# Kernel tuning notes

Measured on AMD Instinct MI355X. Metric: run time of the kernel, lower is better.

## Reference

```python
import jax, jax.numpy as jnp
import numpy as np

B, S, D, H = 2, 2048, 1024, 16
DH = D // H


def setup_inputs() -> dict:
    key = jax.random.key(0)
    ks_ = jax.random.split(key, 12)
    s = 1.0 / np.sqrt(D)
    return {
        "qs": jax.random.normal(ks_[0], (B, S, D), jnp.float32),
        "ks": jax.random.normal(ks_[1], (B, S, D), jnp.float32),
        "vs": jax.random.normal(ks_[2], (B, S, D), jnp.float32),
        "mask": jax.random.randint(ks_[3], (B, S), 0, 2) > 0,
        "Wq": jax.random.normal(ks_[4], (D, D), jnp.float32) * s,
        "bq": jnp.zeros((D,), jnp.float32),
        "Wk": jax.random.normal(ks_[5], (D, D), jnp.float32) * s,
        "bk": jnp.zeros((D,), jnp.float32),
        "Wv": jax.random.normal(ks_[6], (D, D), jnp.float32) * s,
        "bv": jnp.zeros((D,), jnp.float32),
        "Wo": jax.random.normal(ks_[7], (D, D), jnp.float32) * s,
        "bo": jnp.zeros((D,), jnp.float32),
    }


def reference(qs, ks, vs, mask, Wq, bq, Wk, bk, Wv, bv, Wo, bo):
    # Linear projections (single-layer MLPs)
    q = qs @ Wq + bq  # [B,S,D]
    k = ks @ Wk + bk
    v = vs @ Wv + bv
    # split heads: B L (H D) -> B H L D
    split = lambda x: x.reshape(B, S, H, DH).transpose(0, 2, 1, 3)
    q, k, v = split(q), split(k), split(v)
    scores = jnp.einsum("bhqd,bhkd->bhqk", q, k) / jnp.sqrt(jnp.float32(DH))
    scores = jnp.where(mask[:, None, None, :], scores, -jnp.inf)
    attn = jax.nn.softmax(scores, axis=-1)  # [B,H,Q,K]
    ctx = jnp.einsum("bhqk,bhkd->bhqd", attn, v)
    ctx = ctx.transpose(0, 2, 1, 3).reshape(B, S, D)  # B H L D -> B L (H D)
    out = ctx @ Wo + bo
    return (out, attn)
```

## Files before the change

kernel.cpp:

```cpp
#include <hip/hip_runtime.h>
#include <hip/hip_bf16.h>
#include <cstdint>

#define NBATCH 2
#define NS 2048
#define NDIM 1024
#define NHEAD 16
#define NDH 64
#define NBH 32

typedef __bf16 bf16x8 __attribute__((ext_vector_type(8)));
typedef float f32x4 __attribute__((ext_vector_type(4)));

#define QK_EXP2_SCALE 0.1803368801111244f

#define WAITV(N) asm volatile("s_waitcnt vmcnt(" #N ")" ::: "memory")
#define FENCE asm volatile("" ::: "memory")

static __device__ __forceinline__ f32x4 mfma16(bf16x8 a, bf16x8 b, f32x4 c) {
  return __builtin_amdgcn_mfma_f32_16x16x32_bf16(a, b, c, 0, 0, 0);
}

static __device__ __forceinline__ void gload_lds16(const void* g, void* l) {
  __builtin_amdgcn_global_load_lds(
      (const __attribute__((address_space(1))) uint32_t*)g,
      (__attribute__((address_space(3))) uint32_t*)l, 16, 0, 0);
}

__global__ __launch_bounds__(256) void k_cvt_x(const float* __restrict__ q,
                                               const float* __restrict__ k,
                                               const float* __restrict__ v,
                                               __bf16* __restrict__ out) {
  const float* src = blockIdx.y == 0 ? q : (blockIdx.y == 1 ? k : v);
  __bf16* dst = out + (size_t)blockIdx.y * (size_t)(4096 * 1024);
  int i = blockIdx.x * 256 + threadIdx.x;
  const float4* s4 = reinterpret_cast<const float4*>(src) + (size_t)i * 2;
  float4 a = s4[0], b = s4[1];
  bf16x8 o;
  o[0] = (__bf16)a.x; o[1] = (__bf16)a.y; o[2] = (__bf16)a.z; o[3] = (__bf16)a.w;
  o[4] = (__bf16)b.x; o[5] = (__bf16)b.y; o[6] = (__bf16)b.z; o[7] = (__bf16)b.w;
  *reinterpret_cast<bf16x8*>(dst + (size_t)i * 8) = o;
}

__global__ __launch_bounds__(256) void k_cvt_w(const float* __restrict__ Wq,
                                               const float* __restrict__ Wk,
                                               const float* __restrict__ Wv,
                                               const float* __restrict__ Wo,
                                               __bf16* __restrict__ out,
                                               const int* __restrict__ mask,
                                               float* __restrict__ biasf) {
  if (blockIdx.y == 4) {
    int t = blockIdx.x * 256 + threadIdx.x;
    if (t < NBATCH * NS) biasf[t] = mask[t] ? 0.f : -1e30f;
    return;
  }
  const float* W = blockIdx.y == 0 ? Wq : (blockIdx.y == 1 ? Wk
                   : (blockIdx.y == 2 ? Wv : Wo));
  __bf16* dst = out + (size_t)blockIdx.y * (size_t)(1024 * 1024);
  int t = blockIdx.x * 256 + threadIdx.x;
  int n = t & 1023;
  int kc = t >> 10;
  bf16x8 o;
#pragma unroll
  for (int j = 0; j < 8; ++j) o[j] = (__bf16)W[(size_t)(kc * 8 + j) * 1024 + n];
  *reinterpret_cast<bf16x8*>(dst + (size_t)n * 1024 + kc * 8) = o;
}

__global__ __launch_bounds__(256) void k_tr_v(const __bf16* __restrict__ V,
                                              __bf16* __restrict__ Vt) {
  int t = blockIdx.x * 256 + threadIdx.x;
  int d = t & 63;
  int sc = (t >> 6) & 255;
  int bh = t >> 14;
  bf16x8 o;
#pragma unroll
  for (int j = 0; j < 8; ++j)
    o[j] = V[((size_t)bh * 2048 + sc * 8 + j) * 64 + d];
  *reinterpret_cast<bf16x8*>(Vt + ((size_t)bh * 64 + d) * 2048 + sc * 8) = o;
}

__global__ __launch_bounds__(256) void k_gemm(const __bf16* __restrict__ Abase,
                                              const __bf16* __restrict__ Btbase,
                                              const float* __restrict__ b0,
                                              const float* __restrict__ b1,
                                              const float* __restrict__ b2,
                                              void* __restrict__ outbase,
                                              int mode) {
  __shared__ __align__(16) char smem[65536];
  const int job = blockIdx.y;
  const __bf16* A = Abase + (size_t)job * (size_t)(4096 * 1024);
  const __bf16* Bt = Btbase + (size_t)job * (size_t)(1024 * 1024);
  const float* bias = job == 0 ? b0 : (job == 1 ? b1 : b2);
  const int x = blockIdx.x;
  const int mt = (x & 7) * 4 + (x >> 6);
  const int nt = (x >> 3) & 7;
  const int tid = threadIdx.x;
  const int w = tid >> 6, l = tid & 63;
  const int wr = w >> 1, wc = w & 1;

  auto stage = [&](int buf, int kt) {
    const int k0 = kt * 64;
    char* al = smem + buf * 32768;
    char* bl = al + 16384;
#pragma unroll
    for (int i = 0; i < 4; ++i) {
      int ch = tid + i * 256;
      int r = ch >> 3, c = ch & 7;
      int cs = c ^ (r & 7);
      gload_lds16(A + (size_t)(mt * 128 + r) * 1024 + k0 + cs * 8, al + ch * 16);
      gload_lds16(Bt + (size_t)(nt * 128 + r) * 1024 + k0 + cs * 8, bl + ch * 16);
    }
  };

  f32x4 acc[4][4] = {};
  stage(0, 0);
  for (int kt = 0; kt < 16; ++kt) {
    __syncthreads();
    if (kt + 1 < 16) stage((kt + 1) & 1, kt + 1);
    const char* al = smem + (kt & 1) * 32768;
    const char* bl = al + 16384;
#pragma unroll
    for (int ks = 0; ks < 2; ++ks) {
      bf16x8 af[4], bfr[4];
#pragma unroll
      for (int i = 0; i < 4; ++i) {
        int ra = wr * 64 + i * 16 + (l & 15);
        int ca = (ks * 4 + (l >> 4)) ^ (ra & 7);
        af[i] = *reinterpret_cast<const bf16x8*>(al + ra * 128 + ca * 16);
        int rb = wc * 64 + i * 16 + (l & 15);
        int cb = (ks * 4 + (l >> 4)) ^ (rb & 7);
        bfr[i] = *reinterpret_cast<const bf16x8*>(bl + rb * 128 + cb * 16);
      }
#pragma unroll
      for (int mi = 0; mi < 4; ++mi)
#pragma unroll
        for (int ni = 0; ni < 4; ++ni)
          acc[mi][ni] = mfma16(af[mi], bfr[ni], acc[mi][ni]);
    }
  }

  if (mode == 0) {
    const float sc = (job == 0) ? QK_EXP2_SCALE : 1.0f;
    __bf16* outp = (__bf16*)outbase + (size_t)job * (size_t)(NBH * NS * NDH);
#pragma unroll
    for (int mi = 0; mi < 4; ++mi)
#pragma unroll
      for (int ni = 0; ni < 4; ++ni)
#pragma unroll
        for (int r = 0; r < 4; ++r) {
          int m = mt * 128 + wr * 64 + mi * 16 + (l >> 4) * 4 + r;
          int n = nt * 128 + wc * 64 + ni * 16 + (l & 15);
          float v = (acc[mi][ni][r] + bias[n]) * sc;
          int b = m >> 11, s = m & 2047, h = n >> 6, d = n & 63;
          outp[(((size_t)(b * 16 + h)) * 2048 + s) * 64 + d] = (__bf16)v;
        }
  } else {
    float* outp = (float*)outbase;
#pragma unroll
    for (int mi = 0; mi < 4; ++mi)
#pragma unroll
      for (int ni = 0; ni < 4; ++ni)
#pragma unroll
        for (int r = 0; r < 4; ++r) {
          int m = mt * 128 + wr * 64 + mi * 16 + (l >> 4) * 4 + r;
          int n = nt * 128 + wc * 64 + ni * 16 + (l & 15);
          outp[(size_t)m * 1024 + n] = acc[mi][ni][r] + bias[n];
        }
  }
}

__global__ __launch_bounds__(256, 2) void k_attn(
    const __bf16* __restrict__ Qw, const __bf16* __restrict__ Kw,
    const __bf16* __restrict__ Vt, const float* __restrict__ biasf,
    float* __restrict__ attn_out, __bf16* __restrict__ ctx_out) {
  __shared__ __align__(16) char smem[75264];
  const int wg = blockIdx.x;
  const int swz = (wg & 7) * 64 + (wg >> 3);
  const int qt = swz & 15;
  const int bh = swz >> 4;
  const int b = bh >> 4;
  const int tid = threadIdx.x, w = tid >> 6, l = tid & 63;
  const int g = l >> 4, c = l & 15;
  const int qw = qt * 128 + w * 32;
  const float* biasb = biasf + b * 2048;

  bf16x8 qa[2][2];
#pragma unroll
  for (int mi = 0; mi < 2; ++mi)
#pragma unroll
    for (int ks = 0; ks < 2; ++ks)
      qa[mi][ks] = *reinterpret_cast<const bf16x8*>(
          Qw + ((size_t)bh * 2048 + qw + mi * 16 + c) * 64 + ks * 32 + g * 8);

  auto stageK = [&](char* dst, int kt) {
#pragma unroll
    for (int i = 0; i < 4; ++i) {
      int ch = tid + i * 256;
      int r = ch >> 3, cc = ch & 7;
      int cs = cc ^ (r & 7);
      gload_lds16(Kw + ((size_t)bh * 2048 + kt * 128 + r) * 64 + cs * 8,
                  dst + ch * 16);
    }
  };
  auto stageV = [&](char* dst, int kt) {
#pragma unroll
    for (int i = 0; i < 4; ++i) {
      int ch = tid + i * 256;
      int r = ch >> 4, cc = ch & 15;
      int cs = cc ^ (r & 15);
      gload_lds16(Vt + ((size_t)bh * 64 + r) * 2048 + kt * 128 + cs * 8,
                  dst + ch * 16);
    }
  };
  auto stageBias = [&](int slot, int kt) {
    if (l < 32)
      gload_lds16(biasb + kt * 128 + l * 4, smem + 73728 + slot * 512);
  };

  float rs[2] = {0.f, 0.f};
  stageK(smem, 0);
  stageBias(0, 0);
  int sl = 0;
  for (int kt = 0; kt < 16; ++kt) {
    int nx = (sl + 1 == 3) ? 0 : sl + 1;
    if (kt + 1 < 16) {
      stageK(smem + nx * 16384, kt + 1);
      stageBias(nx, kt + 1);
      WAITV(5);
    } else {
      WAITV(0);
    }
    __builtin_amdgcn_s_barrier();
    FENCE;
    const char* kl = smem + sl * 16384;
    const float* bl = (const float*)(smem + 73728 + sl * 512);
#pragma unroll
    for (int nb = 0; nb < 8; ++nb) {
      bf16x8 kb[2];
#pragma unroll
      for (int ks = 0; ks < 2; ++ks) {
        int r = nb * 16 + c;
        int cc = (ks * 4 + g) ^ (r & 7);
        kb[ks] = *reinterpret_cast<const bf16x8*>(kl + r * 128 + cc * 16);
      }
      f32x4 cinit = *reinterpret_cast<const f32x4*>(bl + nb * 16 + g * 4);
#pragma unroll
      for (int mi = 0; mi < 2; ++mi) {
        f32x4 s = mfma16(kb[0], qa[mi][0], cinit);
        s = mfma16(kb[1], qa[mi][1], s);
        rs[mi] += exp2f(s[0]) + exp2f(s[1]) + exp2f(s[2]) + exp2f(s[3]);
      }
    }
    sl = nx;
  }
  float inv_[2];
#pragma unroll
  for (int mi = 0; mi < 2; ++mi) {
    float v = rs[mi];
    v += __shfl_xor(v, 16, 64);
    v += __shfl_xor(v, 32, 64);
    inv_[mi] = v > 0.f ? 1.f / v : 0.f;
  }
  FENCE; __builtin_amdgcn_s_barrier(); FENCE;

  f32x4 ctx[2][4] = {};
  float* attnb = attn_out + (size_t)bh * 2048 * 2048;
  char* pF = smem + 65536 + w * 2048;
  stageK(smem, 0);
  stageV(smem + 32768, 0);
  stageBias(0, 0);
  for (int kt = 0; kt < 16; ++kt) {
    if (kt + 1 < 16) {
      int nx3 = (kt + 1) % 3;
      stageK(smem + ((kt + 1) & 1) * 16384, kt + 1);
      stageV(smem + 32768 + ((kt + 1) & 1) * 16384, kt + 1);
      stageBias(nx3, kt + 1);
    }
    if (kt == 0) WAITV(9);
    else if (kt == 15) WAITV(16);
    else WAITV(25);
    FENCE; __builtin_amdgcn_s_barrier(); FENCE;
    const char* kl = smem + (kt & 1) * 16384;
    const char* vl = smem + 32768 + (kt & 1) * 16384;
    const float* bl = (const float*)(smem + 73728 + (kt % 3) * 512);
#pragma unroll
    for (int kc = 0; kc < 4; ++kc) {
      bf16x8 kbj[2][2];
      f32x4 cin[2];
#pragma unroll
      for (int j = 0; j < 2; ++j) {
        const int nb = kc * 2 + j;
#pragma unroll
        for (int ks = 0; ks < 2; ++ks) {
          int r = nb * 16 + c;
          int cc = (ks * 4 + g) ^ (r & 7);
          kbj[j][ks] = *reinterpret_cast<const bf16x8*>(kl + r * 128 + cc * 16);
        }
        cin[j] = *reinterpret_cast<const f32x4*>(bl + nb * 16 + g * 4);
      }
      bf16x8 vb[4];
#pragma unroll
      for (int nd = 0; nd < 4; ++nd) {
        int dd = nd * 16 + c;
        int ch = (kc * 4 + g) ^ (dd & 15);
        vb[nd] = *reinterpret_cast<const bf16x8*>(vl + dd * 256 + ch * 16);
      }
#pragma unroll
      for (int mi = 0; mi < 2; ++mi) {
#pragma unroll
        for (int j = 0; j < 2; ++j) {
          f32x4 s = mfma16(kbj[j][0], qa[mi][0], cin[j]);
          s = mfma16(kbj[j][1], qa[mi][1], s);
          f32x4 p;
#pragma unroll
          for (int r = 0; r < 4; ++r) p[r] = exp2f(s[r]) * inv_[mi];
          *reinterpret_cast<f32x4*>(
              pF + c * 128 + (((j * 4 + g) ^ (c & 7)) * 16)) = p;
        }
        bf16x8 pa;
        {
          f32x4 lo = *reinterpret_cast<const f32x4*>(
              pF + c * 128 + (((2 * g) ^ (c & 7)) * 16));
          f32x4 hi = *reinterpret_cast<const f32x4*>(
              pF + c * 128 + (((2 * g + 1) ^ (c & 7)) * 16));
          pa[0] = (__bf16)lo[0]; pa[1] = (__bf16)lo[1];
          pa[2] = (__bf16)lo[2]; pa[3] = (__bf16)lo[3];
          pa[4] = (__bf16)hi[0]; pa[5] = (__bf16)hi[1];
          pa[6] = (__bf16)hi[2]; pa[7] = (__bf16)hi[3];
        }
#pragma unroll
        for (int nd = 0; nd < 4; ++nd)
          ctx[mi][nd] = mfma16(pa, vb[nd], ctx[mi][nd]);
#pragma unroll
        for (int u = 0; u < 2; ++u) {
          int rr = u * 8 + (l >> 3);
          int ch = (l & 7) ^ (rr & 7);
          f32x4 pv = *reinterpret_cast<const f32x4*>(pF + rr * 128 + ch * 16);
          *reinterpret_cast<f32x4*>(
              attnb + (size_t)(qw + mi * 16 + rr) * 2048 + kt * 128 +
              kc * 32 + (l & 7) * 4) = pv;
        }
      }
    }
    FENCE; __builtin_amdgcn_s_barrier(); FENCE;
  }

  const int h = bh & 15;
#pragma unroll
  for (int mi = 0; mi < 2; ++mi)
#pragma unroll
    for (int nd = 0; nd < 4; ++nd)
#pragma unroll
      for (int r = 0; r < 4; ++r) {
        int m = b * 2048 + qw + mi * 16 + g * 4 + r;
        int n = h * 64 + nd * 16 + c;
        ctx_out[(size_t)m * 1024 + n] = (__bf16)ctx[mi][nd][r];
      }
}

extern "C" void kernel_launch(void* const* d_in, const int* in_sizes, int n_in,
                              void* d_out, int out_size, void* d_ws,
                              size_t ws_size, hipStream_t stream) {
  const float* qs = (const float*)d_in[0];
  const float* ks = (const float*)d_in[1];
  const float* vs = (const float*)d_in[2];
  const int* mask = (const int*)d_in[3];
  const float* Wq = (const float*)d_in[4];
  const float* bq = (const float*)d_in[5];
  const float* Wk = (const float*)d_in[6];
  const float* bk = (const float*)d_in[7];
  const float* Wv = (const float*)d_in[8];
  const float* bv = (const float*)d_in[9];
  const float* Wo = (const float*)d_in[10];
  const float* bo = (const float*)d_in[11];

  char* ws = (char*)d_ws;
  __bf16* Xb = (__bf16*)(ws);
  __bf16* Wt = (__bf16*)(ws + 25165824);
  __bf16* QKV = (__bf16*)(ws + 58720256);
  float* biasf = (float*)(ws + 83886080);
  __bf16* Vt = (__bf16*)(ws);
  __bf16* ctx = (__bf16*)(ws + 8388608);
  float* out = (float*)d_out;
  float* attn = out + (size_t)4194304;

  k_cvt_x<<<dim3(2048, 3), 256, 0, stream>>>(qs, ks, vs, Xb);
  k_cvt_w<<<dim3(512, 5), 256, 0, stream>>>(Wq, Wk, Wv, Wo, Wt, mask, biasf);
  k_gemm<<<dim3(256, 3), 256, 0, stream>>>(Xb, Wt, bq, bk, bv, QKV, 0);
  k_tr_v<<<dim3(2048), 256, 0, stream>>>(QKV + (size_t)2 * 4194304, Vt);
  k_attn<<<dim3(512), 256, 0, stream>>>(QKV, QKV + (size_t)4194304, Vt, biasf,
                                        attn, ctx);
  k_gemm<<<dim3(256, 1), 256, 0, stream>>>(ctx, Wt + (size_t)3 * 1048576, bo,
                                           bo, bo, d_out, 1);
}
```

Before: 239.9 us.

## Use 8 waves per attention block with 16 query rows each

The attention kernel moves from 4 waves handling 32 query rows each to 8 waves handling 16 rows each. Staging loads are split across 512 threads, and the per-wave P buffer is widened to a full 128-key row. Attention-probability stores are now batched once per key tile instead of once per 32-key chunk. Bigger LDS use (about 130KB) and launch_bounds(512,1) allow one block per CU, so the gain in wave-level parallelism is traded against fewer concurrent blocks and more K/V LDS reads per output.

```diff
diff --git a/kernel.cpp b/kernel.cpp
--- a/kernel.cpp
+++ b/kernel.cpp
@@ -169,11 +169,11 @@
   }
 }
 
-__global__ __launch_bounds__(256, 2) void k_attn(
+__global__ __launch_bounds__(512, 1) void k_attn(
     const __bf16* __restrict__ Qw, const __bf16* __restrict__ Kw,
     const __bf16* __restrict__ Vt, const float* __restrict__ biasf,
     float* __restrict__ attn_out, __bf16* __restrict__ ctx_out) {
-  __shared__ __align__(16) char smem[75264];
+  __shared__ __align__(16) char smem[132608];
   const int wg = blockIdx.x;
   const int swz = (wg & 7) * 64 + (wg >> 3);
   const int qt = swz & 15;
@@ -181,21 +181,19 @@
   const int b = bh >> 4;
   const int tid = threadIdx.x, w = tid >> 6, l = tid & 63;
   const int g = l >> 4, c = l & 15;
-  const int qw = qt * 128 + w * 32;
+  const int qw = qt * 128 + w * 16;
   const float* biasb = biasf + b * 2048;
 
-  bf16x8 qa[2][2];
-#pragma unroll
-  for (int mi = 0; mi < 2; ++mi)
-#pragma unroll
-    for (int ks = 0; ks < 2; ++ks)
-      qa[mi][ks] = *reinterpret_cast<const bf16x8*>(
-          Qw + ((size_t)bh * 2048 + qw + mi * 16 + c) * 64 + ks * 32 + g * 8);
+  bf16x8 qa[2];
+#pragma unroll
+  for (int ks = 0; ks < 2; ++ks)
+    qa[ks] = *reinterpret_cast<const bf16x8*>(
+        Qw + ((size_t)bh * 2048 + qw + c) * 64 + ks * 32 + g * 8);
 
   auto stageK = [&](char* dst, int kt) {
 #pragma unroll
-    for (int i = 0; i < 4; ++i) {
-      int ch = tid + i * 256;
+    for (int i = 0; i < 2; ++i) {
+      int ch = tid + i * 512;
       int r = ch >> 3, cc = ch & 7;
       int cs = cc ^ (r & 7);
       gload_lds16(Kw + ((size_t)bh * 2048 + kt * 128 + r) * 64 + cs * 8,
@@ -204,8 +202,8 @@
   };
   auto stageV = [&](char* dst, int kt) {
 #pragma unroll
-    for (int i = 0; i < 4; ++i) {
-      int ch = tid + i * 256;
+    for (int i = 0; i < 2; ++i) {
+      int ch = tid + i * 512;
       int r = ch >> 4, cc = ch & 15;
       int cs = cc ^ (r & 15);
       gload_lds16(Vt + ((size_t)bh * 64 + r) * 2048 + kt * 128 + cs * 8,
@@ -214,10 +212,10 @@
   };
   auto stageBias = [&](int slot, int kt) {
     if (l < 32)
-      gload_lds16(biasb + kt * 128 + l * 4, smem + 73728 + slot * 512);
+      gload_lds16(biasb + kt * 128 + l * 4, smem + 131072 + slot * 512);
   };
 
-  float rs[2] = {0.f, 0.f};
+  float rs = 0.f;
   stageK(smem, 0);
   stageBias(0, 0);
   int sl = 0;
@@ -226,14 +224,14 @@
     if (kt + 1 < 16) {
       stageK(smem + nx * 16384, kt + 1);
       stageBias(nx, kt + 1);
-      WAITV(5);
+      WAITV(3);
     } else {
       WAITV(0);
     }
     __builtin_amdgcn_s_barrier();
     FENCE;
     const char* kl = smem + sl * 16384;
-    const float* bl = (const float*)(smem + 73728 + sl * 512);
+    const float* bl = (const float*)(smem + 131072 + sl * 512);
 #pragma unroll
     for (int nb = 0; nb < 8; ++nb) {
       bf16x8 kb[2];
@@ -244,59 +242,71 @@
         kb[ks] = *reinterpret_cast<const bf16x8*>(kl + r * 128 + cc * 16);
       }
       f32x4 cinit = *reinterpret_cast<const f32x4*>(bl + nb * 16 + g * 4);
-#pragma unroll
-      for (int mi = 0; mi < 2; ++mi) {
-        f32x4 s = mfma16(kb[0], qa[mi][0], cinit);
-        s = mfma16(kb[1], qa[mi][1], s);
-        rs[mi] += exp2f(s[0]) + exp2f(s[1]) + exp2f(s[2]) + exp2f(s[3]);
-      }
+      f32x4 s = mfma16(kb[0], qa[0], cinit);
+      s = mfma16(kb[1], qa[1], s);
+      rs += exp2f(s[0]) + exp2f(s[1]) + exp2f(s[2]) + exp2f(s[3]);
     }
     sl = nx;
   }
-  float inv_[2];
-#pragma unroll
-  for (int mi = 0; mi < 2; ++mi) {
-    float v = rs[mi];
+  float inv_;
+  {
+    float v = rs;
     v += __shfl_xor(v, 16, 64);
     v += __shfl_xor(v, 32, 64);
-    inv_[mi] = v > 0.f ? 1.f / v : 0.f;
+    inv_ = v > 0.f ? 1.f / v : 0.f;
   }
   FENCE; __builtin_amdgcn_s_barrier(); FENCE;
 
-  f32x4 ctx[2][4] = {};
+  f32x4 ctx[4] = {};
   float* attnb = attn_out + (size_t)bh * 2048 * 2048;
-  char* pF = smem + 65536 + w * 2048;
+  char* pF = smem + 65536 + w * 8192;
   stageK(smem, 0);
   stageV(smem + 32768, 0);
   stageBias(0, 0);
   for (int kt = 0; kt < 16; ++kt) {
     if (kt + 1 < 16) {
-      int nx3 = (kt + 1) % 3;
       stageK(smem + ((kt + 1) & 1) * 16384, kt + 1);
       stageV(smem + 32768 + ((kt + 1) & 1) * 16384, kt + 1);
-      stageBias(nx3, kt + 1);
-    }
-    if (kt == 0) WAITV(9);
-    else if (kt == 15) WAITV(16);
-    else WAITV(25);
+      stageBias((kt + 1) & 1, kt + 1);
+    }
+    if (kt == 0) WAITV(5);
+    else if (kt == 15) WAITV(8);
+    else WAITV(13);
     FENCE; __builtin_amdgcn_s_barrier(); FENCE;
     const char* kl = smem + (kt & 1) * 16384;
     const char* vl = smem + 32768 + (kt & 1) * 16384;
-    const float* bl = (const float*)(smem + 73728 + (kt % 3) * 512);
+    const float* bl = (const float*)(smem + 131072 + (kt & 1) * 512);
 #pragma unroll
     for (int kc = 0; kc < 4; ++kc) {
-      bf16x8 kbj[2][2];
-      f32x4 cin[2];
 #pragma unroll
       for (int j = 0; j < 2; ++j) {
         const int nb = kc * 2 + j;
+        bf16x8 kb[2];
 #pragma unroll
         for (int ks = 0; ks < 2; ++ks) {
           int r = nb * 16 + c;
           int cc = (ks * 4 + g) ^ (r & 7);
-          kbj[j][ks] = *reinterpret_cast<const bf16x8*>(kl + r * 128 + cc * 16);
+          kb[ks] = *reinterpret_cast<const bf16x8*>(kl + r * 128 + cc * 16);
         }
-        cin[j] = *reinterpret_cast<const f32x4*>(bl + nb * 16 + g * 4);
+        f32x4 cinit = *reinterpret_cast<const f32x4*>(bl + nb * 16 + g * 4);
+        f32x4 s = mfma16(kb[0], qa[0], cinit);
+        s = mfma16(kb[1], qa[1], s);
+        f32x4 p;
+#pragma unroll
+        for (int r = 0; r < 4; ++r) p[r] = exp2f(s[r]) * inv_;
+        *reinterpret_cast<f32x4*>(
+            pF + c * 512 + (((nb * 4 + g) ^ (c & 7)) * 16)) = p;
+      }
+      bf16x8 pa;
+      {
+        f32x4 lo = *reinterpret_cast<const f32x4*>(
+            pF + c * 512 + (((kc * 8 + g * 2) ^ (c & 7)) * 16));
+        f32x4 hi = *reinterpret_cast<const f32x4*>(
+            pF + c * 512 + (((kc * 8 + g * 2 + 1) ^ (c & 7)) * 16));
+        pa[0] = (__bf16)lo[0]; pa[1] = (__bf16)lo[1];
+        pa[2] = (__bf16)lo[2]; pa[3] = (__bf16)lo[3];
+        pa[4] = (__bf16)hi[0]; pa[5] = (__bf16)hi[1];
+        pa[6] = (__bf16)hi[2]; pa[7] = (__bf16)hi[3];
       }
       bf16x8 vb[4];
 #pragma unroll
@@ -306,40 +316,19 @@
         vb[nd] = *reinterpret_cast<const bf16x8*>(vl + dd * 256 + ch * 16);
       }
 #pragma unroll
-      for (int mi = 0; mi < 2; ++mi) {
-#pragma unroll
-        for (int j = 0; j < 2; ++j) {
-          f32x4 s = mfma16(kbj[j][0], qa[mi][0], cin[j]);
-          s = mfma16(kbj[j][1], qa[mi][1], s);
-          f32x4 p;
-#pragma unroll
-          for (int r = 0; r < 4; ++r) p[r] = exp2f(s[r]) * inv_[mi];
-          *reinterpret_cast<f32x4*>(
-              pF + c * 128 + (((j * 4 + g) ^ (c & 7)) * 16)) = p;
-        }
-        bf16x8 pa;
-        {
-          f32x4 lo = *reinterpret_cast<const f32x4*>(
-              pF + c * 128 + (((2 * g) ^ (c & 7)) * 16));
-          f32x4 hi = *reinterpret_cast<const f32x4*>(
-              pF + c * 128 + (((2 * g + 1) ^ (c & 7)) * 16));
-          pa[0] = (__bf16)lo[0]; pa[1] = (__bf16)lo[1];
-          pa[2] = (__bf16)lo[2]; pa[3] = (__bf16)lo[3];
-          pa[4] = (__bf16)hi[0]; pa[5] = (__bf16)hi[1];
-          pa[6] = (__bf16)hi[2]; pa[7] = (__bf16)hi[3];
-        }
-#pragma unroll
-        for (int nd = 0; nd < 4; ++nd)
-          ctx[mi][nd] = mfma16(pa, vb[nd], ctx[mi][nd]);
-#pragma unroll
-        for (int u = 0; u < 2; ++u) {
-          int rr = u * 8 + (l >> 3);
-          int ch = (l & 7) ^ (rr & 7);
-          f32x4 pv = *reinterpret_cast<const f32x4*>(pF + rr * 128 + ch * 16);
-          *reinterpret_cast<f32x4*>(
-              attnb + (size_t)(qw + mi * 16 + rr) * 2048 + kt * 128 +
-              kc * 32 + (l & 7) * 4) = pv;
-        }
+      for (int nd = 0; nd < 4; ++nd)
+        ctx[nd] = mfma16(pa, vb[nd], ctx[nd]);
+    }
+#pragma unroll
+    for (int rg = 0; rg < 2; ++rg) {
+      const int row = rg * 8 + (l >> 3);
+#pragma unroll
+      for (int cc = 0; cc < 4; ++cc) {
+        int chunk = (cc * 8 + (l & 7)) ^ (row & 7);
+        f32x4 pv = *reinterpret_cast<const f32x4*>(pF + row * 512 + chunk * 16);
+        *reinterpret_cast<f32x4*>(
+            attnb + (size_t)(qw + row) * 2048 + kt * 128 + cc * 32 +
+            (l & 7) * 4) = pv;
       }
     }
     FENCE; __builtin_amdgcn_s_barrier(); FENCE;
@@ -347,15 +336,13 @@
 
   const int h = bh & 15;
 #pragma unroll
-  for (int mi = 0; mi < 2; ++mi)
-#pragma unroll
-    for (int nd = 0; nd < 4; ++nd)
-#pragma unroll
-      for (int r = 0; r < 4; ++r) {
-        int m = b * 2048 + qw + mi * 16 + g * 4 + r;
-        int n = h * 64 + nd * 16 + c;
-        ctx_out[(size_t)m * 1024 + n] = (__bf16)ctx[mi][nd][r];
-      }
+  for (int nd = 0; nd < 4; ++nd)
+#pragma unroll
+    for (int r = 0; r < 4; ++r) {
+      int m = b * 2048 + qw + g * 4 + r;
+      int n = h * 64 + nd * 16 + c;
+      ctx_out[(size_t)m * 1024 + n] = (__bf16)ctx[nd][r];
+    }
 }
 
 extern "C" void kernel_launch(void* const* d_in, const int* in_sizes, int n_in,
@@ -388,7 +375,7 @@
   k_cvt_w<<<dim3(512, 5), 256, 0, stream>>>(Wq, Wk, Wv, Wo, Wt, mask, biasf);
   k_gemm<<<dim3(256, 3), 256, 0, stream>>>(Xb, Wt, bq, bk, bv, QKV, 0);
   k_tr_v<<<dim3(2048), 256, 0, stream>>>(QKV + (size_t)2 * 4194304, Vt);
-  k_attn<<<dim3(512), 256, 0, stream>>>(QKV, QKV + (size_t)4194304, Vt, biasf,
+  k_attn<<<dim3(512), 512, 0, stream>>>(QKV, QKV + (size_t)4194304, Vt, biasf,
                                         attn, ctx);
   k_gemm<<<dim3(256, 1), 256, 0, stream>>>(ctx, Wt + (size_t)3 * 1048576, bo,
                                            bo, bo, d_out, 1);
```

After: 250.5 us. 4.4% more time.
